# Optimization experiments

Hardware: AMD Instinct MI355X
Metric: run time of the kernel (lower is better)

The kernel has to match this reference:

```python
import jax, jax.numpy as jnp
import numpy as np

B, V_IN, V_OUT, F_IN, F_OUT, N_CP = 100000, 128, 128, 512, 512, 16
DIM_H = max(V_IN, V_OUT)  # hidden_vectors=None -> max(dim_vectors_in, dim_vectors_out)
EPS = 1e-8


def setup_inputs() -> dict:
    key = jax.random.key(0)
    ks = jax.random.split(key, 9)
    u = lambda k, shape, scale: jax.random.uniform(k, shape, jnp.float32, -scale, scale)
    wh_k = 1.0 / np.sqrt(V_IN).astype(np.float32)
    wu_k = 1.0 / np.sqrt(DIM_H + N_CP).astype(np.float32)
    f_in = DIM_H + N_CP + F_IN  # 656
    kf = 1.0 / np.sqrt(f_in).astype(np.float32)
    kg = 1.0 / np.sqrt(F_OUT).astype(np.float32)
    return {
        "feats": jax.random.normal(ks[0], (B, F_IN), jnp.float32),
        "vectors": jax.random.normal(ks[1], (B, V_IN, 3), jnp.float32),
        "Wh": u(ks[2], (V_IN, DIM_H), wh_k),
        "Wcp": u(ks[3], (V_IN, 2 * N_CP), wh_k),
        "Wu": u(ks[4], (DIM_H + N_CP, V_OUT), wu_k),
        "Wf": u(ks[5], (f_in, F_OUT), kf),      # torch Linear weight, stored (in,out)
        "bf": u(ks[6], (F_OUT,), kf),
        "Wg": u(ks[7], (F_OUT, V_OUT), kg),
        "bg": u(ks[8], (V_OUT,), kg),
    }


def reference(feats, vectors, Wh, Wcp, Wu, Wf, bf, Wg, bg):
    # vectors: [b, v_in, 3]; mix vector channels (matmul acts per xyz component c)
    Vh = jnp.einsum('bvc,vh->bhc', vectors, Wh)            # [b, dim_h, 3]
    # cross-product features
    Vcp = jnp.einsum('bvc,vp->bpc', vectors, Wcp)          # [b, 2*n_cp, 3]
    cp = jnp.cross(Vcp[:, :N_CP], Vcp[:, N_CP:])           # [b, n_cp, 3]
    Vh = jnp.concatenate([Vh, cp], axis=1)                 # [b, dim_h+n_cp, 3]
    Vu = jnp.einsum('bkc,ko->boc', Vh, Wu)                 # [b, v_out, 3]
    # clamped L2 norm over xyz
    sh = jnp.sqrt(jnp.maximum(jnp.sum(Vh * Vh, axis=-1), EPS))  # [b, dim_h+n_cp]
    s = jnp.concatenate([feats, sh], axis=1)               # [b, dim_h+n_cp+f_in]
    feats_out = jax.nn.silu(s @ Wf + bf)                   # [b, f_out]
    gating = feats_out @ Wg + bg                           # [b, v_out]
    vectors_out = jax.nn.sigmoid(gating)[..., None] * Vu   # [b, v_out, 3]
    return feats_out, vectors_out
```

## Files before the change

### kernel.cpp

```cpp
#include <hip/hip_runtime.h>

#define BATCH 100000
#define M3 300000
#define VECBASE 51200000
#define KP 704

typedef float fl4  __attribute__((ext_vector_type(4)));
typedef float f32x4 __attribute__((ext_vector_type(4)));
typedef short s16x8 __attribute__((ext_vector_type(8)));

__device__ __forceinline__ short f2bf(float f) {
  unsigned int u = __float_as_uint(f);
  u += 0x7fffu + ((u >> 16) & 1u);
  return (short)(u >> 16);
}
__device__ __forceinline__ float bf2f(short s) {
  return __uint_as_float(((unsigned int)(unsigned short)s) << 16);
}
__device__ __forceinline__ s16x8 pack8(fl4 a, fl4 b) {
  s16x8 o;
  o[0] = f2bf(a[0]); o[1] = f2bf(a[1]); o[2] = f2bf(a[2]); o[3] = f2bf(a[3]);
  o[4] = f2bf(b[0]); o[5] = f2bf(b[1]); o[6] = f2bf(b[2]); o[7] = f2bf(b[3]);
  return o;
}
__device__ __forceinline__ void glds16(const void* g, void* l) {
  __builtin_amdgcn_global_load_lds((const __attribute__((address_space(1))) void*)g,
                                   (__attribute__((address_space(3))) void*)l, 16, 0, 0);
}
#define SWOFF(row, ck) (((row) << 5) + ((((ck) ^ (((row) >> 1) & 3))) << 3))

__global__ __launch_bounds__(256) void prep_w(
    const float* __restrict__ Wh, const float* __restrict__ Wcp,
    const float* __restrict__ Wu, const float* __restrict__ Wf,
    const float* __restrict__ Wg, short* __restrict__ WB1,
    short* __restrict__ WuTp, short* __restrict__ WfT, short* __restrict__ WgT) {
  int gid = blockIdx.x * 256 + threadIdx.x;
  if (gid < 20480) {
    int n = gid >> 7, k = gid & 127;
    WB1[gid] = f2bf(n < 128 ? Wh[k * 128 + n] : Wcp[k * 32 + (n - 128)]);
  } else if (gid < 40960) {
    int i = gid - 20480;
    int o = i / 160, k = i - o * 160;
    WuTp[i] = k < 144 ? f2bf(Wu[k * 128 + o]) : (short)0;
  } else if (gid < 40960 + 512 * KP) {
    int i = gid - 40960;
    int n = i / KP, k = i - n * KP;
    WfT[i] = k < 656 ? f2bf(Wf[k * 512 + n]) : (short)0;
  } else if (gid < 40960 + 512 * KP + 65536) {
    int i = gid - (40960 + 512 * KP);
    int n = i >> 9, k = i & 511;
    WgT[i] = f2bf(Wg[k * 128 + n]);
  }
}

__global__ __launch_bounds__(256) void geo_gemm1(
    const float* __restrict__ vecs, const short* __restrict__ WB1,
    short* __restrict__ Vcat, short* __restrict__ sh192) {
  __shared__ __align__(16) short U[192 * 160];
  const int t = threadIdx.x;
  const int b0 = blockIdx.x * 64;
  const int row0 = blockIdx.x * 192;

#pragma unroll
  for (int it = 0; it < 24; ++it) {
    int fj = (it * 256 + t) * 4;
    int bl = fj / 384;
    int rem = fj - bl * 384;
    int v = rem / 3, c = rem - v * 3;
    fl4 val = (fl4){0.f, 0.f, 0.f, 0.f};
    int b = b0 + bl;
    if (b < BATCH) val = *reinterpret_cast<const fl4*>(&vecs[(size_t)b * 384 + rem]);
#pragma unroll
    for (int e = 0; e < 4; ++e) {
      int row = bl * 3 + c;
      int off = (row << 8) + (v << 1);
      *(short*)((char*)U + (off ^ ((row & 7) << 4))) = f2bf(val[e]);
      if (++c == 3) { c = 0; ++v; }
    }
  }
  __syncthreads();

  const int lane = t & 63, wv = t >> 6;
  const int wr = wv >> 1, wc = wv & 1;
  const int lr = lane & 15, lk = lane >> 4;
  f32x4 acc[6][5];
#pragma unroll
  for (int i = 0; i < 6; ++i)
#pragma unroll
    for (int j = 0; j < 5; ++j) acc[i][j] = (f32x4){0.f, 0.f, 0.f, 0.f};

#pragma unroll
  for (int kk = 0; kk < 4; ++kk) {
    s16x8 af[6], bq[5];
#pragma unroll
    for (int mi = 0; mi < 6; ++mi) {
      int row = wr * 96 + mi * 16 + lr;
      int off = (row << 8) + (kk << 6) + (lk << 4);
      af[mi] = *(const s16x8*)((const char*)U + (off ^ ((row & 7) << 4)));
    }
#pragma unroll
    for (int ni = 0; ni < 5; ++ni)
      bq[ni] = *reinterpret_cast<const s16x8*>(
          &WB1[(wc * 80 + ni * 16 + lr) * 128 + (kk << 5) + (lk << 3)]);
#pragma unroll
    for (int mi = 0; mi < 6; ++mi)
#pragma unroll
      for (int ni = 0; ni < 5; ++ni)
        acc[mi][ni] = __builtin_amdgcn_mfma_f32_16x16x32_bf16(af[mi], bq[ni], acc[mi][ni], 0, 0, 0);
  }
  __syncthreads();

#pragma unroll
  for (int mi = 0; mi < 6; ++mi)
#pragma unroll
    for (int ni = 0; ni < 5; ++ni) {
      int col = wc * 80 + ni * 16 + lr;
#pragma unroll
      for (int r = 0; r < 4; ++r) {
        int row = wr * 96 + mi * 16 + lk * 4 + r;
        U[row * 160 + col] = f2bf(acc[mi][ni][r]);
      }
    }
  __syncthreads();

  {
    int bl = t >> 2, pj = t & 3;
    int gb = b0 + bl;
    float shcp[4];
#pragma unroll
    for (int q = 0; q < 4; ++q) {
      int p = pj * 4 + q;
      float ax = bf2f(U[(bl * 3 + 0) * 160 + 128 + p]);
      float ay = bf2f(U[(bl * 3 + 1) * 160 + 128 + p]);
      float az = bf2f(U[(bl * 3 + 2) * 160 + 128 + p]);
      float bx = bf2f(U[(bl * 3 + 0) * 160 + 144 + p]);
      float by = bf2f(U[(bl * 3 + 1) * 160 + 144 + p]);
      float bz = bf2f(U[(bl * 3 + 2) * 160 + 144 + p]);
      float cx = ay * bz - az * by;
      float cy = az * bx - ax * bz;
      float cz = ax * by - ay * bx;
      U[(bl * 3 + 0) * 160 + 128 + p] = f2bf(cx);
      U[(bl * 3 + 1) * 160 + 128 + p] = f2bf(cy);
      U[(bl * 3 + 2) * 160 + 128 + p] = f2bf(cz);
      U[(bl * 3 + 0) * 160 + 144 + p] = 0;
      U[(bl * 3 + 1) * 160 + 144 + p] = 0;
      U[(bl * 3 + 2) * 160 + 144 + p] = 0;
      shcp[q] = sqrtf(fmaxf(cx * cx + cy * cy + cz * cz, 1e-8f));
    }
    if (gb < BATCH) {
#pragma unroll
      for (int q = 0; q < 4; ++q) sh192[(size_t)gb * 192 + 128 + pj * 4 + q] = f2bf(shcp[q]);
#pragma unroll
      for (int z = 0; z < 12; ++z) sh192[(size_t)gb * 192 + 144 + pj * 12 + z] = 0;
    }
  }
  {
    int bl = t >> 2, kq = t & 3;
    int gb = b0 + bl;
    if (gb < BATCH) {
#pragma unroll
      for (int j = 0; j < 4; ++j) {
        int k = kq * 32 + j * 8;
        s16x8 r0 = *(const s16x8*)&U[(bl * 3 + 0) * 160 + k];
        s16x8 r1 = *(const s16x8*)&U[(bl * 3 + 1) * 160 + k];
        s16x8 r2 = *(const s16x8*)&U[(bl * 3 + 2) * 160 + k];
        s16x8 o;
#pragma unroll
        for (int e = 0; e < 8; ++e) {
          float x = bf2f(r0[e]), y = bf2f(r1[e]), z = bf2f(r2[e]);
          o[e] = f2bf(sqrtf(fmaxf(x * x + y * y + z * z, 1e-8f)));
        }
        *(s16x8*)&sh192[(size_t)gb * 192 + k] = o;
      }
    }
  }
  __syncthreads();
  {
    const char* src = (const char*)U;
    char* dst = (char*)Vcat + (size_t)row0 * 320;
    size_t lim = 96000000ULL - (size_t)row0 * 320;
#pragma unroll
    for (int j = 0; j < 15; ++j) {
      int byte = (j * 256 + t) * 16;
      if ((size_t)byte < lim)
        *(s16x8*)(dst + byte) = *(const s16x8*)(src + byte);
    }
  }
}

__global__ __launch_bounds__(256) void geo_gemm2(
    const short* __restrict__ Vcat, const short* __restrict__ WuTp,
    short* __restrict__ Vub) {
  __shared__ __align__(16) short Al[128 * 192];
  const int t = threadIdx.x;
  const int row0 = blockIdx.x << 7;
#pragma unroll
  for (int it = 0; it < 10; ++it) {
    int idx = it * 256 + t;
    int r = idx / 20, ch = idx - r * 20;
    int grow = row0 + r;
    s16x8 q = (s16x8){0, 0, 0, 0, 0, 0, 0, 0};
    if (grow < M3) q = *reinterpret_cast<const s16x8*>(&Vcat[(size_t)grow * 160 + ch * 8]);
    int off = r * 384 + ch * 16;
    *(s16x8*)((char*)Al + (off ^ ((r & 7) << 4))) = q;
  }
  __syncthreads();

  const int lane = t & 63, wv = t >> 6;
  const int wr = wv >> 1, wc = wv & 1;
  const int lr = lane & 15, lk = lane >> 4;
  f32x4 acc[4][4];
#pragma unroll
  for (int i = 0; i < 4; ++i)
#pragma unroll
    for (int j = 0; j < 4; ++j) acc[i][j] = (f32x4){0.f, 0.f, 0.f, 0.f};

#pragma unroll
  for (int kk = 0; kk < 5; ++kk) {
    s16x8 af[4], bq[4];
#pragma unroll
    for (int mi = 0; mi < 4; ++mi) {
      int row = wr * 64 + mi * 16 + lr;
      int off = row * 384 + (kk << 6) + (lk << 4);
      af[mi] = *(const s16x8*)((const char*)Al + (off ^ ((row & 7) << 4)));
    }
#pragma unroll
    for (int ni = 0; ni < 4; ++ni)
      bq[ni] = *reinterpret_cast<const s16x8*>(
          &WuTp[(wc * 64 + ni * 16 + lr) * 160 + (kk << 5) + (lk << 3)]);
#pragma unroll
    for (int mi = 0; mi < 4; ++mi)
#pragma unroll
      for (int ni = 0; ni < 4; ++ni)
        acc[mi][ni] = __builtin_amdgcn_mfma_f32_16x16x32_bf16(af[mi], bq[ni], acc[mi][ni], 0, 0, 0);
  }
#pragma unroll
  for (int mi = 0; mi < 4; ++mi)
#pragma unroll
    for (int ni = 0; ni < 4; ++ni) {
      int col = wc * 64 + ni * 16 + lr;
#pragma unroll
      for (int r = 0; r < 4; ++r) {
        int row = row0 + wr * 64 + mi * 16 + lk * 4 + r;
        if (row < M3) Vub[(size_t)row * 128 + col] = f2bf(acc[mi][ni][r]);
      }
    }
}

__global__ __launch_bounds__(256) void gemm_feats(
    const float* __restrict__ feats, const short* __restrict__ sh192,
    const short* __restrict__ WfT, const float* __restrict__ bfv,
    float* __restrict__ out) {
  const int bid = blockIdx.x;
  const int swz = (bid & 7) * 391 + (bid >> 3);
  const int mt = swz >> 2, nt = swz & 3;
  const int row0 = mt << 7, n0 = nt << 7;
  const int t = threadIdx.x;
  const int lane = t & 63, wv = t >> 6;
  const int wr = wv >> 1, wc = wv & 1;
  const int lr = lane & 15, lk = lane >> 4;

  __shared__ __align__(16) short Al[2][128 * 32];
  __shared__ __align__(16) short Bl[2][128 * 32];

  const int ar = t >> 1, h = t & 1;
  const size_t arowc = (size_t)min(row0 + ar, BATCH - 1);
  const float* aFp = &feats[arowc * 512 + h * 16];
  const short* aSp = &sh192[arowc * 192 + h * 16];
  const int aw1 = SWOFF(ar, 2 * h), aw2 = SWOFF(ar, 2 * h + 1);

  const int bc = (lane & 3) ^ ((lane >> 3) & 3);
  const short* bSrc0 = &WfT[(size_t)(n0 + (wv * 2 + 0) * 16 + (lane >> 2)) * KP + bc * 8];
  const short* bSrc1 = &WfT[(size_t)(n0 + (wv * 2 + 1) * 16 + (lane >> 2)) * KP + bc * 8];

  f32x4 acc[4][4];
#pragma unroll
  for (int i = 0; i < 4; ++i)
#pragma unroll
    for (int j = 0; j < 4; ++j) acc[i][j] = (f32x4){0.f, 0.f, 0.f, 0.f};

  fl4 frA[4], frB[4];
  s16x8 sA0, sA1, sB0, sB1;

  auto issueA = [&](int ks, fl4* fr, s16x8& s0, s16x8& s1) {
    const int k0 = ks << 5;
    if (k0 < 512) {
#pragma unroll
      for (int j = 0; j < 4; ++j) fr[j] = *reinterpret_cast<const fl4*>(aFp + k0 + j * 4);
    } else {
      s0 = *reinterpret_cast<const s16x8*>(aSp + (k0 - 512));
      s1 = *reinterpret_cast<const s16x8*>(aSp + (k0 - 512) + 8);
    }
  };
  auto commitA = [&](int ks, int buf, const fl4* fr, const s16x8& s0, const s16x8& s1) {
    s16x8 lo, hi;
    if ((ks << 5) < 512) { lo = pack8(fr[0], fr[1]); hi = pack8(fr[2], fr[3]); }
    else { lo = s0; hi = s1; }
    *(s16x8*)&Al[buf][aw1] = lo;
    *(s16x8*)&Al[buf][aw2] = hi;
  };
  auto gldsB = [&](int ks, int buf) {
    const int k0 = ks << 5;
    glds16(bSrc0 + k0, &Bl[buf][(wv * 2 + 0) * 512]);
    glds16(bSrc1 + k0, &Bl[buf][(wv * 2 + 1) * 512]);
  };
  auto compute = [&](int buf) {
    s16x8 af[4], bq[4];
#pragma unroll
    for (int mi = 0; mi < 4; ++mi) {
      int rw = wr * 64 + mi * 16 + lr;
      af[mi] = *(const s16x8*)&Al[buf][SWOFF(rw, lk)];
    }
#pragma unroll
    for (int ni = 0; ni < 4; ++ni) {
      int rw = wc * 64 + ni * 16 + lr;
      bq[ni] = *(const s16x8*)&Bl[buf][SWOFF(rw, lk)];
    }
#pragma unroll
    for (int mi = 0; mi < 4; ++mi)
#pragma unroll
      for (int ni = 0; ni < 4; ++ni)
        acc[mi][ni] = __builtin_amdgcn_mfma_f32_16x16x32_bf16(af[mi], bq[ni], acc[mi][ni], 0, 0, 0);
  };

  issueA(0, frA, sA0, sA1);
  commitA(0, 0, frA, sA0, sA1);
  gldsB(0, 0);
  issueA(1, frB, sB0, sB1);
  __syncthreads();

  for (int ks = 0; ks < 22; ks += 2) {
    if (ks + 2 < 22) issueA(ks + 2, frA, sA0, sA1);
    if (ks + 1 < 22) { commitA(ks + 1, 1, frB, sB0, sB1); gldsB(ks + 1, 1); }
    compute(0);
    __syncthreads();
    if (ks + 3 < 22) issueA(ks + 3, frB, sB0, sB1);
    if (ks + 2 < 22) { commitA(ks + 2, 0, frA, sA0, sA1); gldsB(ks + 2, 0); }
    if (ks + 1 < 22) compute(1);
    __syncthreads();
  }

#pragma unroll
  for (int ni = 0; ni < 4; ++ni) {
    int col = n0 + wc * 64 + ni * 16 + lr;
    float bb = bfv[col];
#pragma unroll
    for (int mi = 0; mi < 4; ++mi) {
      int rbase = row0 + wr * 64 + mi * 16 + lk * 4;
#pragma unroll
      for (int rr = 0; rr < 4; ++rr) {
        int gr = rbase + rr;
        if (gr < BATCH) {
          float x = acc[mi][ni][rr] + bb;
          out[(size_t)gr * 512 + col] = x / (1.f + __expf(-x));
        }
      }
    }
  }
}

__global__ __launch_bounds__(256) void gemm_gate(
    const float* __restrict__ fo, const short* __restrict__ WgT,
    const float* __restrict__ bg, const short* __restrict__ Vub,
    float* __restrict__ out) {
  const int bid = blockIdx.x;
  const int xcd = bid & 7, bidx = bid >> 3;
  const int swz = (xcd < 6 ? xcd * 98 : 6 * 98 + (xcd - 6) * 97) + bidx;
  const int row0 = swz << 7;
  const int t = threadIdx.x;
  const int lane = t & 63, wv = t >> 6;
  const int wr = wv >> 1, wc = wv & 1;
  const int lr = lane & 15, lk = lane >> 4;

  __shared__ __align__(16) short Al[2][128 * 32];
  __shared__ __align__(16) short Bl[2][128 * 32];

  const int ar = t >> 1, h = t & 1;
  const size_t arowc = (size_t)min(row0 + ar, BATCH - 1);
  const float* aFp = &fo[arowc * 512 + h * 16];
  const int aw1 = SWOFF(ar, 2 * h), aw2 = SWOFF(ar, 2 * h + 1);

  const int bc = (lane & 3) ^ ((lane >> 3) & 3);
  const short* bSrc0 = &WgT[(size_t)((wv * 2 + 0) * 16 + (lane >> 2)) * 512 + bc * 8];
  const short* bSrc1 = &WgT[(size_t)((wv * 2 + 1) * 16 + (lane >> 2)) * 512 + bc * 8];

  f32x4 acc[4][4];
#pragma unroll
  for (int i = 0; i < 4; ++i)
#pragma unroll
    for (int j = 0; j < 4; ++j) acc[i][j] = (f32x4){0.f, 0.f, 0.f, 0.f};

  fl4 frA[4], frB[4];

  auto issueA = [&](int ks, fl4* fr) {
    const int k0 = ks << 5;
#pragma unroll
    for (int j = 0; j < 4; ++j) fr[j] = *reinterpret_cast<const fl4*>(aFp + k0 + j * 4);
  };
  auto commitA = [&](int buf, const fl4* fr) {
    *(s16x8*)&Al[buf][aw1] = pack8(fr[0], fr[1]);
    *(s16x8*)&Al[buf][aw2] = pack8(fr[2], fr[3]);
  };
  auto gldsB = [&](int ks, int buf) {
    const int k0 = ks << 5;
    glds16(bSrc0 + k0, &Bl[buf][(wv * 2 + 0) * 512]);
    glds16(bSrc1 + k0, &Bl[buf][(wv * 2 + 1) * 512]);
  };
  auto compute = [&](int buf) {
    s16x8 af[4], bq[4];
#pragma unroll
    for (int mi = 0; mi < 4; ++mi) {
      int rw = wr * 64 + mi * 16 + lr;
      af[mi] = *(const s16x8*)&Al[buf][SWOFF(rw, lk)];
    }
#pragma unroll
    for (int ni = 0; ni < 4; ++ni) {
      int rw = wc * 64 + ni * 16 + lr;
      bq[ni] = *(const s16x8*)&Bl[buf][SWOFF(rw, lk)];
    }
#pragma unroll
    for (int mi = 0; mi < 4; ++mi)
#pragma unroll
      for (int ni = 0; ni < 4; ++ni)
        acc[mi][ni] = __builtin_amdgcn_mfma_f32_16x16x32_bf16(af[mi], bq[ni], acc[mi][ni], 0, 0, 0);
  };

  issueA(0, frA);
  commitA(0, frA);
  gldsB(0, 0);
  issueA(1, frB);
  __syncthreads();

  for (int ks = 0; ks < 16; ks += 2) {
    if (ks + 2 < 16) issueA(ks + 2, frA);
    if (ks + 1 < 16) { commitA(1, frB); gldsB(ks + 1, 1); }
    compute(0);
    __syncthreads();
    if (ks + 3 < 16) issueA(ks + 3, frB);
    if (ks + 2 < 16) { commitA(0, frA); gldsB(ks + 2, 0); }
    if (ks + 1 < 16) compute(1);
    __syncthreads();
  }

#pragma unroll
  for (int ni = 0; ni < 4; ++ni) {
    int col = wc * 64 + ni * 16 + lr;
    float bb = bg[col];
#pragma unroll
    for (int mi = 0; mi < 4; ++mi) {
      int rbase = row0 + wr * 64 + mi * 16 + lk * 4;
#pragma unroll
      for (int rr = 0; rr < 4; ++rr) {
        int gr = rbase + rr;
        if (gr < BATCH) {
          float x = acc[mi][ni][rr] + bb;
          float gate = 1.f / (1.f + __expf(-x));
          size_t vb = (size_t)(3 * gr) * 128 + col;
          float* po = &out[VECBASE + ((size_t)gr * 128 + col) * 3];
          po[0] = gate * bf2f(Vub[vb]);
          po[1] = gate * bf2f(Vub[vb + 128]);
          po[2] = gate * bf2f(Vub[vb + 256]);
        }
      }
    }
  }
}

extern "C" void kernel_launch(void* const* d_in, const int* in_sizes, int n_in,
                              void* d_out, int out_size, void* d_ws, size_t ws_size,
                              hipStream_t stream) {
  const float* feats = (const float*)d_in[0];
  const float* vecs  = (const float*)d_in[1];
  const float* Wh    = (const float*)d_in[2];
  const float* Wcp   = (const float*)d_in[3];
  const float* Wu    = (const float*)d_in[4];
  const float* Wf    = (const float*)d_in[5];
  const float* bfv   = (const float*)d_in[6];
  const float* Wg    = (const float*)d_in[7];
  const float* bg    = (const float*)d_in[8];
  float* out = (float*)d_out;

  char* ws = (char*)d_ws;
  short* sh192 = (short*)ws;
  short* Vub   = (short*)(ws + 38400000);
  short* WfT   = (short*)(ws + 115200000);
  short* WgT   = (short*)(ws + 115920896);
  short* WB1   = (short*)(ws + 116051968);
  short* WuTp  = (short*)(ws + 116092928);

  short* Vcat = (short*)d_out;

  hipLaunchKernelGGL(prep_w,     dim3(1824), dim3(256), 0, stream, Wh, Wcp, Wu, Wf, Wg, WB1, WuTp, WfT, WgT);
  hipLaunchKernelGGL(geo_gemm1,  dim3(1563), dim3(256), 0, stream, vecs, WB1, Vcat, sh192);
  hipLaunchKernelGGL(geo_gemm2,  dim3(2344), dim3(256), 0, stream, Vcat, WuTp, Vub);
  hipLaunchKernelGGL(gemm_feats, dim3(3128), dim3(256), 0, stream, feats, sh192, WfT, bfv, out);
  hipLaunchKernelGGL(gemm_gate,  dim3(782),  dim3(256), 0, stream, out, WgT, bg, Vub, out);
}
```

Baseline: 523.6 us.

## Pre-convert feats into combined bf16 A matrix and simplify feats GEMM loop

geo_gemm1 now also converts the fp32 feats rows to bf16 and writes them, together with the norm features, into one contiguous row-major A buffer of width KP. gemm_feats then loads both A and B tiles with direct global-to-LDS loads instead of register loads plus packing, but drops the double-buffered software pipeline and LDS swizzle in favour of a single buffer with two barriers per k-step. The aim is to halve A-side read traffic across the four column tiles and remove conversion work from the GEMM. The cost is an extra write and read of a 140 MB intermediate, less overlap between loads and MFMA, and possible LDS bank conflicts.

```diff
diff --git a/kernel.cpp b/kernel.cpp
--- a/kernel.cpp
+++ b/kernel.cpp
@@ -54,8 +54,9 @@
 }
 
 __global__ __launch_bounds__(256) void geo_gemm1(
-    const float* __restrict__ vecs, const short* __restrict__ WB1,
-    short* __restrict__ Vcat, short* __restrict__ sh192) {
+    const float* __restrict__ vecs, const float* __restrict__ feats,
+    const short* __restrict__ WB1, short* __restrict__ Vcat,
+    short* __restrict__ Ab) {
   __shared__ __align__(16) short U[192 * 160];
   const int t = threadIdx.x;
   const int b0 = blockIdx.x * 64;
@@ -149,9 +150,11 @@
     }
     if (gb < BATCH) {
 #pragma unroll
-      for (int q = 0; q < 4; ++q) sh192[(size_t)gb * 192 + 128 + pj * 4 + q] = f2bf(shcp[q]);
-#pragma unroll
-      for (int z = 0; z < 12; ++z) sh192[(size_t)gb * 192 + 144 + pj * 12 + z] = 0;
+      for (int q = 0; q < 4; ++q)
+        Ab[(size_t)gb * KP + 512 + 128 + pj * 4 + q] = f2bf(shcp[q]);
+#pragma unroll
+      for (int z = 0; z < 12; ++z)
+        Ab[(size_t)gb * KP + 512 + 144 + pj * 12 + z] = 0;
     }
   }
   {
@@ -170,7 +173,7 @@
           float x = bf2f(r0[e]), y = bf2f(r1[e]), z = bf2f(r2[e]);
           o[e] = f2bf(sqrtf(fmaxf(x * x + y * y + z * z, 1e-8f)));
         }
-        *(s16x8*)&sh192[(size_t)gb * 192 + k] = o;
+        *(s16x8*)&Ab[(size_t)gb * KP + 512 + k] = o;
       }
     }
   }
@@ -184,6 +187,19 @@
       int byte = (j * 256 + t) * 16;
       if ((size_t)byte < lim)
         *(s16x8*)(dst + byte) = *(const s16x8*)(src + byte);
+    }
+  }
+  {
+#pragma unroll
+    for (int j = 0; j < 16; ++j) {
+      int idx = (j * 256 + t) * 8;
+      int bl = idx >> 9, kk = idx & 511;
+      int gb = b0 + bl;
+      if (gb < BATCH) {
+        fl4 v0 = *(const fl4*)&feats[(size_t)gb * 512 + kk];
+        fl4 v1 = *(const fl4*)&feats[(size_t)gb * 512 + kk + 4];
+        *(s16x8*)&Ab[(size_t)gb * KP + kk] = pack8(v0, v1);
+      }
     }
   }
 }
@@ -248,9 +264,8 @@
 }
 
 __global__ __launch_bounds__(256) void gemm_feats(
-    const float* __restrict__ feats, const short* __restrict__ sh192,
-    const short* __restrict__ WfT, const float* __restrict__ bfv,
-    float* __restrict__ out) {
+    const short* __restrict__ Ab, const short* __restrict__ WfT,
+    const float* __restrict__ bfv, float* __restrict__ out) {
   const int bid = blockIdx.x;
   const int swz = (bid & 7) * 391 + (bid >> 3);
   const int mt = swz >> 2, nt = swz & 3;
@@ -260,18 +275,14 @@
   const int wr = wv >> 1, wc = wv & 1;
   const int lr = lane & 15, lk = lane >> 4;
 
-  __shared__ __align__(16) short Al[2][128 * 32];
-  __shared__ __align__(16) short Bl[2][128 * 32];
-
-  const int ar = t >> 1, h = t & 1;
-  const size_t arowc = (size_t)min(row0 + ar, BATCH - 1);
-  const float* aFp = &feats[arowc * 512 + h * 16];
-  const short* aSp = &sh192[arowc * 192 + h * 16];
-  const int aw1 = SWOFF(ar, 2 * h), aw2 = SWOFF(ar, 2 * h + 1);
-
-  const int bc = (lane & 3) ^ ((lane >> 3) & 3);
-  const short* bSrc0 = &WfT[(size_t)(n0 + (wv * 2 + 0) * 16 + (lane >> 2)) * KP + bc * 8];
-  const short* bSrc1 = &WfT[(size_t)(n0 + (wv * 2 + 1) * 16 + (lane >> 2)) * KP + bc * 8];
+  __shared__ __align__(16) short As[128 * 32];
+  __shared__ __align__(16) short Bs[128 * 32];
+
+  const int srow0 = t >> 2, ck = t & 3;
+  const short* ap1 = &Ab[(size_t)min(row0 + srow0, BATCH - 1) * KP + ck * 8];
+  const short* ap2 = &Ab[(size_t)min(row0 + 64 + srow0, BATCH - 1) * KP + ck * 8];
+  const short* bp1 = &WfT[(size_t)(n0 + srow0) * KP + ck * 8];
+  const short* bp2 = &WfT[(size_t)(n0 + 64 + srow0) * KP + ck * 8];
 
   f32x4 acc[4][4];
 #pragma unroll
@@ -279,65 +290,26 @@
 #pragma unroll
     for (int j = 0; j < 4; ++j) acc[i][j] = (f32x4){0.f, 0.f, 0.f, 0.f};
 
-  fl4 frA[4], frB[4];
-  s16x8 sA0, sA1, sB0, sB1;
-
-  auto issueA = [&](int ks, fl4* fr, s16x8& s0, s16x8& s1) {
+  for (int ks = 0; ks < 22; ++ks) {
     const int k0 = ks << 5;
-    if (k0 < 512) {
-#pragma unroll
-      for (int j = 0; j < 4; ++j) fr[j] = *reinterpret_cast<const fl4*>(aFp + k0 + j * 4);
-    } else {
-      s0 = *reinterpret_cast<const s16x8*>(aSp + (k0 - 512));
-      s1 = *reinterpret_cast<const s16x8*>(aSp + (k0 - 512) + 8);
-    }
-  };
-  auto commitA = [&](int ks, int buf, const fl4* fr, const s16x8& s0, const s16x8& s1) {
-    s16x8 lo, hi;
-    if ((ks << 5) < 512) { lo = pack8(fr[0], fr[1]); hi = pack8(fr[2], fr[3]); }
-    else { lo = s0; hi = s1; }
-    *(s16x8*)&Al[buf][aw1] = lo;
-    *(s16x8*)&Al[buf][aw2] = hi;
-  };
-  auto gldsB = [&](int ks, int buf) {
-    const int k0 = ks << 5;
-    glds16(bSrc0 + k0, &Bl[buf][(wv * 2 + 0) * 512]);
-    glds16(bSrc1 + k0, &Bl[buf][(wv * 2 + 1) * 512]);
-  };
-  auto compute = [&](int buf) {
+    __syncthreads();
+    glds16(ap1 + k0, &As[t * 8]);
+    glds16(ap2 + k0, &As[2048 + t * 8]);
+    glds16(bp1 + k0, &Bs[t * 8]);
+    glds16(bp2 + k0, &Bs[2048 + t * 8]);
+    __syncthreads();
     s16x8 af[4], bq[4];
 #pragma unroll
-    for (int mi = 0; mi < 4; ++mi) {
-      int rw = wr * 64 + mi * 16 + lr;
-      af[mi] = *(const s16x8*)&Al[buf][SWOFF(rw, lk)];
-    }
-#pragma unroll
-    for (int ni = 0; ni < 4; ++ni) {
-      int rw = wc * 64 + ni * 16 + lr;
-      bq[ni] = *(const s16x8*)&Bl[buf][SWOFF(rw, lk)];
-    }
+    for (int mi = 0; mi < 4; ++mi)
+      af[mi] = *(const s16x8*)&As[(wr * 64 + mi * 16 + lr) * 32 + lk * 8];
+#pragma unroll
+    for (int ni = 0; ni < 4; ++ni)
+      bq[ni] = *(const s16x8*)&Bs[(wc * 64 + ni * 16 + lr) * 32 + lk * 8];
 #pragma unroll
     for (int mi = 0; mi < 4; ++mi)
 #pragma unroll
       for (int ni = 0; ni < 4; ++ni)
         acc[mi][ni] = __builtin_amdgcn_mfma_f32_16x16x32_bf16(af[mi], bq[ni], acc[mi][ni], 0, 0, 0);
-  };
-
-  issueA(0, frA, sA0, sA1);
-  commitA(0, 0, frA, sA0, sA1);
-  gldsB(0, 0);
-  issueA(1, frB, sB0, sB1);
-  __syncthreads();
-
-  for (int ks = 0; ks < 22; ks += 2) {
-    if (ks + 2 < 22) issueA(ks + 2, frA, sA0, sA1);
-    if (ks + 1 < 22) { commitA(ks + 1, 1, frB, sB0, sB1); gldsB(ks + 1, 1); }
-    compute(0);
-    __syncthreads();
-    if (ks + 3 < 22) issueA(ks + 3, frB, sB0, sB1);
-    if (ks + 2 < 22) { commitA(ks + 2, 0, frA, sA0, sA1); gldsB(ks + 2, 0); }
-    if (ks + 1 < 22) compute(1);
-    __syncthreads();
   }
 
 #pragma unroll
@@ -481,18 +453,18 @@
   float* out = (float*)d_out;
 
   char* ws = (char*)d_ws;
-  short* sh192 = (short*)ws;
-  short* Vub   = (short*)(ws + 38400000);
-  short* WfT   = (short*)(ws + 115200000);
-  short* WgT   = (short*)(ws + 115920896);
-  short* WB1   = (short*)(ws + 116051968);
-  short* WuTp  = (short*)(ws + 116092928);
+  short* Ab   = (short*)ws;
+  short* Vub  = (short*)(ws + 140800000);
+  short* WfT  = (short*)(ws + 217600000);
+  short* WgT  = (short*)(ws + 218320896);
+  short* WB1  = (short*)(ws + 218451968);
+  short* WuTp = (short*)(ws + 218492928);
 
   short* Vcat = (short*)d_out;
 
   hipLaunchKernelGGL(prep_w,     dim3(1824), dim3(256), 0, stream, Wh, Wcp, Wu, Wf, Wg, WB1, WuTp, WfT, WgT);
-  hipLaunchKernelGGL(geo_gemm1,  dim3(1563), dim3(256), 0, stream, vecs, WB1, Vcat, sh192);
+  hipLaunchKernelGGL(geo_gemm1,  dim3(1563), dim3(256), 0, stream, vecs, feats, WB1, Vcat, Ab);
   hipLaunchKernelGGL(geo_gemm2,  dim3(2344), dim3(256), 0, stream, Vcat, WuTp, Vub);
-  hipLaunchKernelGGL(gemm_feats, dim3(3128), dim3(256), 0, stream, feats, sh192, WfT, bfv, out);
+  hipLaunchKernelGGL(gemm_feats, dim3(3128), dim3(256), 0, stream, Ab, WfT, bfv, out);
   hipLaunchKernelGGL(gemm_gate,  dim3(782),  dim3(256), 0, stream, out, WgT, bg, Vub, out);
 }
```

Result: slower. 545.1 us (+4.1%).
